# Kernel tuning notes

Hardware: AMD Instinct MI355X
Metric: run time of the kernel (lower is better)

The kernel has to match this reference:

```python
import jax, jax.numpy as jnp
import numpy as np

B, D_IN, D_H = 8192, 1024, 1024


def setup_inputs() -> dict:
    key = jax.random.key(0)
    ks = jax.random.split(key, 11)
    s_in = 1.0 / np.sqrt(D_IN)
    s_h = 1.0 / np.sqrt(D_H)
    return {
        "x": jax.random.normal(ks[0], (B, D_IN), jnp.float32),
        "h": jax.random.normal(ks[1], (B, D_H), jnp.float32),
        "Wiz": jax.random.normal(ks[2], (D_IN, D_H), jnp.float32) * s_in,
        "Uhz": jax.random.normal(ks[3], (D_H, D_H), jnp.float32) * s_h,
        "bz": jax.random.normal(ks[4], (D_H,), jnp.float32) * 0.01,
        "Wir": jax.random.normal(ks[5], (D_IN, D_H), jnp.float32) * s_in,
        "Uhr": jax.random.normal(ks[6], (D_H, D_H), jnp.float32) * s_h,
        "br": jax.random.normal(ks[7], (D_H,), jnp.float32) * 0.01,
        "Win": jax.random.normal(ks[8], (D_IN, D_H), jnp.float32) * s_in,
        "Uhn": jax.random.normal(ks[9], (D_H, D_H), jnp.float32) * s_h,
        "bn": jax.random.normal(ks[10], (D_H,), jnp.float32) * 0.01,
    }


def reference(x, h, Wiz, Uhz, bz, Wir, Uhr, br, Win, Uhn, bn):
    # Concatenate input-side weights into one GEMM for efficiency; math identical.
    Wi = jnp.concatenate([Wiz, Wir, Win], axis=1)          # [D_in, 3H]
    xz, xr, xn = jnp.split(x @ Wi, 3, axis=1)              # each [B, H]
    Uh = jnp.concatenate([Uhz, Uhr], axis=1)               # [H, 2H]
    hz, hr = jnp.split(h @ Uh, 2, axis=1)
    z = jax.nn.sigmoid(xz + hz + bz)
    r = jax.nn.sigmoid(xr + hr + br)
    # Faithful to source: (r * h) @ Uhn, and act1 (sigmoid) for n, not tanh.
    n = jax.nn.sigmoid(xn + (r * h) @ Uhn + bn)
    return (1.0 - z) * h + z * n
```

## Files before the change

### kernel.cpp

```cpp
#include <hip/hip_runtime.h>
#include <hip/hip_bf16.h>

typedef __attribute__((ext_vector_type(8))) short short8;
typedef __attribute__((ext_vector_type(4))) float f32x4;

#define DEV __device__ __forceinline__

DEV float bf2f(unsigned short u) {
    union { unsigned int i; float f; } v;
    v.i = ((unsigned int)u) << 16;
    return v.f;
}
DEV unsigned short f2bf(float f) {
    union { float f; unsigned int i; } v; v.f = f;
    unsigned int r = v.i + 0x7FFFu + ((v.i >> 16) & 1u);
    return (unsigned short)(r >> 16);
}
DEV float sigmoidf_(float x) {
    return 1.0f / (1.0f + __expf(-x));
}

__global__ void conv_xh(const float* __restrict__ x, const float* __restrict__ h,
                        unsigned short* __restrict__ xw, unsigned short* __restrict__ hw,
                        int n)
{
    int i = (blockIdx.x * blockDim.x + threadIdx.x) * 8;
    const float* src; unsigned short* dst; int off;
    if (i < n) { src = x; dst = xw; off = i; }
    else       { src = h; dst = hw; off = i - n; }
    float4 a = *(const float4*)(src + off);
    float4 b = *(const float4*)(src + off + 4);
    union { uint4 v; unsigned short s[8]; } o;
    o.s[0]=f2bf(a.x); o.s[1]=f2bf(a.y); o.s[2]=f2bf(a.z); o.s[3]=f2bf(a.w);
    o.s[4]=f2bf(b.x); o.s[5]=f2bf(b.y); o.s[6]=f2bf(b.z); o.s[7]=f2bf(b.w);
    *(uint4*)(dst + off) = o.v;
}

__global__ void tconv(const float* __restrict__ s0, const float* __restrict__ s1,
                      const float* __restrict__ s2, const float* __restrict__ s3,
                      const float* __restrict__ s4, const float* __restrict__ s5,
                      unsigned short* __restrict__ d0, unsigned short* __restrict__ d1,
                      unsigned short* __restrict__ d2, unsigned short* __restrict__ d3,
                      unsigned short* __restrict__ d4, unsigned short* __restrict__ d5)
{
    __shared__ float lds[32][33];
    const float* src; unsigned short* dst;
    switch (blockIdx.z) {
        case 0: src=s0; dst=d0; break;
        case 1: src=s1; dst=d1; break;
        case 2: src=s2; dst=d2; break;
        case 3: src=s3; dst=d3; break;
        case 4: src=s4; dst=d4; break;
        default: src=s5; dst=d5; break;
    }
    int k0 = blockIdx.x * 32, n0 = blockIdx.y * 32;
    int tx = threadIdx.x & 31, ty = threadIdx.x >> 5;
    #pragma unroll
    for (int i = 0; i < 4; i++)
        lds[ty + 8*i][tx] = src[(size_t)(k0 + ty + 8*i)*1024 + n0 + tx];
    __syncthreads();
    #pragma unroll
    for (int i = 0; i < 4; i++)
        dst[(size_t)(n0 + ty + 8*i)*1024 + k0 + tx] = f2bf(lds[tx][ty + 8*i]);
}

template<int EPI>
__global__ __launch_bounds__(256, 2)
void gemm_bt(const unsigned short* __restrict__ A,
             const unsigned short* __restrict__ Bt,
             unsigned short* __restrict__ Cbf,
             int N, int K,
             const unsigned short* __restrict__ xn, int xnStride,
             const float* __restrict__ bn,
             const float* __restrict__ zbuf,
             const float* __restrict__ hbuf,
             float* __restrict__ out)
{
    __shared__ unsigned short lA[128*32];
    __shared__ unsigned short lB[128*32];
    const int tid = threadIdx.x;
    const int gm = blockIdx.x * 128, gn = blockIdx.y * 128;

    const int w  = tid >> 6, l = tid & 63;
    const int wm = (w >> 1) * 64, wn = (w & 1) * 64;
    const int lr = l & 15, lk = l >> 4;

    f32x4 acc[4][4] = {};

    const int srow = tid >> 2;
    const int scol = (tid & 3) * 8;
    const unsigned short* Ab = A  + (size_t)(gm + srow) * K + scol;
    const unsigned short* Bb = Bt + (size_t)(gn + srow) * K + scol;
    char* lAp = (char*)lA + tid * 16;
    char* lBp = (char*)lB + tid * 16;

    for (int kt = 0; kt < K; kt += 32) {
        __syncthreads();
        __builtin_amdgcn_global_load_lds(
            (const __attribute__((address_space(1))) void*)(Ab + kt),
            (__attribute__((address_space(3))) void*)lAp, 16, 0, 0);
        __builtin_amdgcn_global_load_lds(
            (const __attribute__((address_space(1))) void*)(Ab + kt + (size_t)64*K),
            (__attribute__((address_space(3))) void*)(lAp + 4096), 16, 0, 0);
        __builtin_amdgcn_global_load_lds(
            (const __attribute__((address_space(1))) void*)(Bb + kt),
            (__attribute__((address_space(3))) void*)lBp, 16, 0, 0);
        __builtin_amdgcn_global_load_lds(
            (const __attribute__((address_space(1))) void*)(Bb + kt + (size_t)64*K),
            (__attribute__((address_space(3))) void*)(lBp + 4096), 16, 0, 0);
        __syncthreads();

        short8 af[4], bfr[4];
        #pragma unroll
        for (int mi = 0; mi < 4; mi++)
            af[mi] = *(const short8*)&lA[(wm + mi*16 + lr)*32 + lk*8];
        #pragma unroll
        for (int ni = 0; ni < 4; ni++)
            bfr[ni] = *(const short8*)&lB[(wn + ni*16 + lr)*32 + lk*8];
        #pragma unroll
        for (int mi = 0; mi < 4; mi++)
            #pragma unroll
            for (int ni = 0; ni < 4; ni++)
                acc[mi][ni] = __builtin_amdgcn_mfma_f32_16x16x32_bf16(
                    af[mi], bfr[ni], acc[mi][ni], 0, 0, 0);
    }

    #pragma unroll
    for (int mi = 0; mi < 4; mi++) {
        #pragma unroll
        for (int j = 0; j < 4; j++) {
            int row = gm + wm + mi*16 + lk*4 + j;
            #pragma unroll
            for (int ni = 0; ni < 4; ni++) {
                int col = gn + wn + ni*16 + lr;
                float v = acc[mi][ni][j];
                if (EPI == 0) {
                    Cbf[(size_t)row * N + col] = f2bf(v);
                } else {
                    float pre = v + bf2f(xn[(size_t)row * xnStride + col]) + bn[col];
                    float nv  = sigmoidf_(pre);
                    float zv  = zbuf[(size_t)row * 1024 + col];
                    float hv  = hbuf[(size_t)row * 1024 + col];
                    out[(size_t)row * 1024 + col] = (1.0f - zv) * hv + zv * nv;
                }
            }
        }
    }
}

__global__ void ew1(const unsigned short* __restrict__ xzrn,
                    const unsigned short* __restrict__ hzr,
                    const float* __restrict__ bz, const float* __restrict__ br,
                    const float* __restrict__ h,
                    float* __restrict__ z, unsigned short* __restrict__ rh)
{
    int i = blockIdx.x * blockDim.x + threadIdx.x;
    int r = i >> 7;
    int c = (i & 127) * 8;
    union { uint4 v; unsigned short s[8]; } xz, xr, hz, hr, rho;
    xz.v = *(const uint4*)(xzrn + (size_t)r*3072 + c);
    xr.v = *(const uint4*)(xzrn + (size_t)r*3072 + 1024 + c);
    hz.v = *(const uint4*)(hzr  + (size_t)r*2048 + c);
    hr.v = *(const uint4*)(hzr  + (size_t)r*2048 + 1024 + c);
    float4 h0 = *(const float4*)(h + (size_t)r*1024 + c);
    float4 h1 = *(const float4*)(h + (size_t)r*1024 + c + 4);
    float hv[8]  = {h0.x,h0.y,h0.z,h0.w,h1.x,h1.y,h1.z,h1.w};
    float4 bz0 = *(const float4*)(bz + c), bz1 = *(const float4*)(bz + c + 4);
    float4 br0 = *(const float4*)(br + c), br1 = *(const float4*)(br + c + 4);
    float bzv[8] = {bz0.x,bz0.y,bz0.z,bz0.w,bz1.x,bz1.y,bz1.z,bz1.w};
    float brv[8] = {br0.x,br0.y,br0.z,br0.w,br1.x,br1.y,br1.z,br1.w};
    float zo[8];
    #pragma unroll
    for (int j = 0; j < 8; j++) {
        float zv = sigmoidf_(bf2f(xz.s[j]) + bf2f(hz.s[j]) + bzv[j]);
        zo[j] = zv;
        float rv = sigmoidf_(bf2f(xr.s[j]) + bf2f(hr.s[j]) + brv[j]);
        rho.s[j] = f2bf(rv * hv[j]);
    }
    *(float4*)(z + (size_t)r*1024 + c)     = make_float4(zo[0],zo[1],zo[2],zo[3]);
    *(float4*)(z + (size_t)r*1024 + c + 4) = make_float4(zo[4],zo[5],zo[6],zo[7]);
    *(uint4*)(rh + (size_t)r*1024 + c) = rho.v;
}

extern "C" void kernel_launch(void* const* d_in, const int* in_sizes, int n_in,
                              void* d_out, int out_size, void* d_ws, size_t ws_size,
                              hipStream_t stream)
{
    const float* x   = (const float*)d_in[0];
    const float* h   = (const float*)d_in[1];
    const float* Wiz = (const float*)d_in[2];
    const float* Uhz = (const float*)d_in[3];
    const float* bz  = (const float*)d_in[4];
    const float* Wir = (const float*)d_in[5];
    const float* Uhr = (const float*)d_in[6];
    const float* br  = (const float*)d_in[7];
    const float* Win = (const float*)d_in[8];
    const float* Uhn = (const float*)d_in[9];
    const float* bn  = (const float*)d_in[10];
    float* out = (float*)d_out;

    char* ws = (char*)d_ws;
    const size_t MB = 1024ull * 1024ull;
    unsigned short* xw   = (unsigned short*)(ws + 0);
    unsigned short* hw   = (unsigned short*)(ws + 16*MB);
    unsigned short* W3t  = (unsigned short*)(ws + 32*MB);
    unsigned short* U2t  = (unsigned short*)(ws + 38*MB);
    unsigned short* Unt  = (unsigned short*)(ws + 42*MB);
    unsigned short* xzrn = (unsigned short*)(ws + 44*MB);
    unsigned short* hzr  = (unsigned short*)(ws + 92*MB);
    float*          zbuf = (float*)(ws + 124*MB);
    unsigned short* rh   = (unsigned short*)(ws + 156*MB);

    const int B = 8192, H = 1024;

    conv_xh<<<dim3(2*B*H/8/256), dim3(256), 0, stream>>>(x, h, xw, hw, B*H);

    tconv<<<dim3(32, 32, 6), dim3(256), 0, stream>>>(
        Wiz, Wir, Win, Uhz, Uhr, Uhn,
        W3t, W3t + 1024*1024, W3t + 2*1024*1024, U2t, U2t + 1024*1024, Unt);

    gemm_bt<0><<<dim3(64, 24), dim3(256), 0, stream>>>(
        xw, W3t, xzrn, 3072, 1024, nullptr, 0, nullptr, nullptr, nullptr, nullptr);

    gemm_bt<0><<<dim3(64, 16), dim3(256), 0, stream>>>(
        hw, U2t, hzr, 2048, 1024, nullptr, 0, nullptr, nullptr, nullptr, nullptr);

    ew1<<<dim3(B*H/8/256), dim3(256), 0, stream>>>(xzrn, hzr, bz, br, h, zbuf, rh);

    gemm_bt<1><<<dim3(64, 8), dim3(256), 0, stream>>>(
        rh, Unt, nullptr, 1024, 1024, xzrn + 2048, 3072, bn, zbuf, h, out);
}
```

Before: 312.8 us.

## Concatenate x/h GEMMs along K and fuse gate elementwise into GEMM epilogues

Stacks input and hidden weights along K so z/r pre-activations come from one K=2048 GEMM with sigmoid and r*h computed in the epilogue, removing the separate elementwise kernel. The n gate is similarly computed as one GEMM over [x | r*h] with stacked Win/Uhn, eliminating the bf16 xzrn/hzr intermediates and their round-trip traffic. Total FLOPs stay the same, but launches and global memory traffic shrink; the epilogue now does branchy per-column work.

Measured after the change: 293.5 us. 1.07x faster.

```diff
diff --git a/kernel.cpp b/kernel.cpp
--- a/kernel.cpp
+++ b/kernel.cpp
@@ -36,22 +36,20 @@
     *(uint4*)(dst + off) = o.v;
 }
 
-__global__ void tconv(const float* __restrict__ s0, const float* __restrict__ s1,
-                      const float* __restrict__ s2, const float* __restrict__ s3,
-                      const float* __restrict__ s4, const float* __restrict__ s5,
-                      unsigned short* __restrict__ d0, unsigned short* __restrict__ d1,
-                      unsigned short* __restrict__ d2, unsigned short* __restrict__ d3,
-                      unsigned short* __restrict__ d4, unsigned short* __restrict__ d5)
+__global__ void tconv(const float* __restrict__ Wiz, const float* __restrict__ Uhz,
+                      const float* __restrict__ Wir, const float* __restrict__ Uhr,
+                      const float* __restrict__ Win, const float* __restrict__ Uhn,
+                      unsigned short* __restrict__ B1t, unsigned short* __restrict__ B3t)
 {
     __shared__ float lds[32][33];
     const float* src; unsigned short* dst;
     switch (blockIdx.z) {
-        case 0: src=s0; dst=d0; break;
-        case 1: src=s1; dst=d1; break;
-        case 2: src=s2; dst=d2; break;
-        case 3: src=s3; dst=d3; break;
-        case 4: src=s4; dst=d4; break;
-        default: src=s5; dst=d5; break;
+        case 0: src=Wiz; dst=B1t;                            break;
+        case 1: src=Uhz; dst=B1t + 1024;                     break;
+        case 2: src=Wir; dst=B1t + (size_t)1024*2048;        break;
+        case 3: src=Uhr; dst=B1t + (size_t)1024*2048 + 1024; break;
+        case 4: src=Win; dst=B3t;                            break;
+        default: src=Uhn; dst=B3t + 1024;                    break;
     }
     int k0 = blockIdx.x * 32, n0 = blockIdx.y * 32;
     int tx = threadIdx.x & 31, ty = threadIdx.x >> 5;
@@ -61,19 +59,19 @@
     __syncthreads();
     #pragma unroll
     for (int i = 0; i < 4; i++)
-        dst[(size_t)(n0 + ty + 8*i)*1024 + k0 + tx] = f2bf(lds[tx][ty + 8*i]);
+        dst[(size_t)(n0 + ty + 8*i)*2048 + k0 + tx] = f2bf(lds[tx][ty + 8*i]);
 }
 
 template<int EPI>
 __global__ __launch_bounds__(256, 2)
-void gemm_bt(const unsigned short* __restrict__ A,
+void gemm_bt(const unsigned short* __restrict__ A0,
+             const unsigned short* __restrict__ A1,
              const unsigned short* __restrict__ Bt,
-             unsigned short* __restrict__ Cbf,
-             int N, int K,
-             const unsigned short* __restrict__ xn, int xnStride,
-             const float* __restrict__ bn,
-             const float* __restrict__ zbuf,
-             const float* __restrict__ hbuf,
+             const float* __restrict__ bias0,
+             const float* __restrict__ bias1,
+             const float* __restrict__ hsrc,
+             float* __restrict__ zbuf,
+             unsigned short* __restrict__ rh,
              float* __restrict__ out)
 {
     __shared__ unsigned short lA[128*32];
@@ -89,24 +87,25 @@
 
     const int srow = tid >> 2;
     const int scol = (tid & 3) * 8;
-    const unsigned short* Ab = A  + (size_t)(gm + srow) * K + scol;
-    const unsigned short* Bb = Bt + (size_t)(gn + srow) * K + scol;
     char* lAp = (char*)lA + tid * 16;
     char* lBp = (char*)lB + tid * 16;
 
-    for (int kt = 0; kt < K; kt += 32) {
+    for (int kt = 0; kt < 2048; kt += 32) {
+        const unsigned short* Ab = (kt < 1024 ? A0 : A1)
+                                 + (size_t)(gm + srow) * 1024 + (kt & 1023) + scol;
+        const unsigned short* Bb = Bt + (size_t)(gn + srow) * 2048 + kt + scol;
         __syncthreads();
         __builtin_amdgcn_global_load_lds(
-            (const __attribute__((address_space(1))) void*)(Ab + kt),
+            (const __attribute__((address_space(1))) void*)Ab,
             (__attribute__((address_space(3))) void*)lAp, 16, 0, 0);
         __builtin_amdgcn_global_load_lds(
-            (const __attribute__((address_space(1))) void*)(Ab + kt + (size_t)64*K),
+            (const __attribute__((address_space(1))) void*)(Ab + (size_t)64*1024),
             (__attribute__((address_space(3))) void*)(lAp + 4096), 16, 0, 0);
         __builtin_amdgcn_global_load_lds(
-            (const __attribute__((address_space(1))) void*)(Bb + kt),
+            (const __attribute__((address_space(1))) void*)Bb,
             (__attribute__((address_space(3))) void*)lBp, 16, 0, 0);
         __builtin_amdgcn_global_load_lds(
-            (const __attribute__((address_space(1))) void*)(Bb + kt + (size_t)64*K),
+            (const __attribute__((address_space(1))) void*)(Bb + (size_t)64*2048),
             (__attribute__((address_space(3))) void*)(lBp + 4096), 16, 0, 0);
         __syncthreads();
 
@@ -134,52 +133,24 @@
             for (int ni = 0; ni < 4; ni++) {
                 int col = gn + wn + ni*16 + lr;
                 float v = acc[mi][ni][j];
-                if (EPI == 0) {
-                    Cbf[(size_t)row * N + col] = f2bf(v);
+                if (EPI == 1) {
+                    if (col < 1024) {
+                        zbuf[(size_t)row*1024 + col] = sigmoidf_(v + bias0[col]);
+                    } else {
+                        int c = col - 1024;
+                        float rv = sigmoidf_(v + bias1[c]);
+                        rh[(size_t)row*1024 + c] =
+                            f2bf(rv * hsrc[(size_t)row*1024 + c]);
+                    }
                 } else {
-                    float pre = v + bf2f(xn[(size_t)row * xnStride + col]) + bn[col];
-                    float nv  = sigmoidf_(pre);
-                    float zv  = zbuf[(size_t)row * 1024 + col];
-                    float hv  = hbuf[(size_t)row * 1024 + col];
-                    out[(size_t)row * 1024 + col] = (1.0f - zv) * hv + zv * nv;
+                    float nv = sigmoidf_(v + bias0[col]);
+                    float zv = zbuf[(size_t)row*1024 + col];
+                    float hv = hsrc[(size_t)row*1024 + col];
+                    out[(size_t)row*1024 + col] = (1.0f - zv)*hv + zv*nv;
                 }
             }
         }
     }
-}
-
-__global__ void ew1(const unsigned short* __restrict__ xzrn,
-                    const unsigned short* __restrict__ hzr,
-                    const float* __restrict__ bz, const float* __restrict__ br,
-                    const float* __restrict__ h,
-                    float* __restrict__ z, unsigned short* __restrict__ rh)
-{
-    int i = blockIdx.x * blockDim.x + threadIdx.x;
-    int r = i >> 7;
-    int c = (i & 127) * 8;
-    union { uint4 v; unsigned short s[8]; } xz, xr, hz, hr, rho;
-    xz.v = *(const uint4*)(xzrn + (size_t)r*3072 + c);
-    xr.v = *(const uint4*)(xzrn + (size_t)r*3072 + 1024 + c);
-    hz.v = *(const uint4*)(hzr  + (size_t)r*2048 + c);
-    hr.v = *(const uint4*)(hzr  + (size_t)r*2048 + 1024 + c);
-    float4 h0 = *(const float4*)(h + (size_t)r*1024 + c);
-    float4 h1 = *(const float4*)(h + (size_t)r*1024 + c + 4);
-    float hv[8]  = {h0.x,h0.y,h0.z,h0.w,h1.x,h1.y,h1.z,h1.w};
-    float4 bz0 = *(const float4*)(bz + c), bz1 = *(const float4*)(bz + c + 4);
-    float4 br0 = *(const float4*)(br + c), br1 = *(const float4*)(br + c + 4);
-    float bzv[8] = {bz0.x,bz0.y,bz0.z,bz0.w,bz1.x,bz1.y,bz1.z,bz1.w};
-    float brv[8] = {br0.x,br0.y,br0.z,br0.w,br1.x,br1.y,br1.z,br1.w};
-    float zo[8];
-    #pragma unroll
-    for (int j = 0; j < 8; j++) {
-        float zv = sigmoidf_(bf2f(xz.s[j]) + bf2f(hz.s[j]) + bzv[j]);
-        zo[j] = zv;
-        float rv = sigmoidf_(bf2f(xr.s[j]) + bf2f(hr.s[j]) + brv[j]);
-        rho.s[j] = f2bf(rv * hv[j]);
-    }
-    *(float4*)(z + (size_t)r*1024 + c)     = make_float4(zo[0],zo[1],zo[2],zo[3]);
-    *(float4*)(z + (size_t)r*1024 + c + 4) = make_float4(zo[4],zo[5],zo[6],zo[7]);
-    *(uint4*)(rh + (size_t)r*1024 + c) = rho.v;
 }
 
 extern "C" void kernel_launch(void* const* d_in, const int* in_sizes, int n_in,
@@ -203,30 +174,21 @@
     const size_t MB = 1024ull * 1024ull;
     unsigned short* xw   = (unsigned short*)(ws + 0);
     unsigned short* hw   = (unsigned short*)(ws + 16*MB);
-    unsigned short* W3t  = (unsigned short*)(ws + 32*MB);
-    unsigned short* U2t  = (unsigned short*)(ws + 38*MB);
-    unsigned short* Unt  = (unsigned short*)(ws + 42*MB);
-    unsigned short* xzrn = (unsigned short*)(ws + 44*MB);
-    unsigned short* hzr  = (unsigned short*)(ws + 92*MB);
-    float*          zbuf = (float*)(ws + 124*MB);
-    unsigned short* rh   = (unsigned short*)(ws + 156*MB);
+    unsigned short* B1t  = (unsigned short*)(ws + 32*MB);
+    unsigned short* B3t  = (unsigned short*)(ws + 40*MB);
+    float*          zbuf = (float*)(ws + 44*MB);
+    unsigned short* rh   = (unsigned short*)(ws + 76*MB);
 
     const int B = 8192, H = 1024;
 
     conv_xh<<<dim3(2*B*H/8/256), dim3(256), 0, stream>>>(x, h, xw, hw, B*H);
 
     tconv<<<dim3(32, 32, 6), dim3(256), 0, stream>>>(
-        Wiz, Wir, Win, Uhz, Uhr, Uhn,
-        W3t, W3t + 1024*1024, W3t + 2*1024*1024, U2t, U2t + 1024*1024, Unt);
+        Wiz, Uhz, Wir, Uhr, Win, Uhn, B1t, B3t);
 
-    gemm_bt<0><<<dim3(64, 24), dim3(256), 0, stream>>>(
-        xw, W3t, xzrn, 3072, 1024, nullptr, 0, nullptr, nullptr, nullptr, nullptr);
+    gemm_bt<1><<<dim3(64, 16), dim3(256), 0, stream>>>(
+        xw, hw, B1t, bz, br, h, zbuf, rh, nullptr);
 
-    gemm_bt<0><<<dim3(64, 16), dim3(256), 0, stream>>>(
-        hw, U2t, hzr, 2048, 1024, nullptr, 0, nullptr, nullptr, nullptr, nullptr);
-
-    ew1<<<dim3(B*H/8/256), dim3(256), 0, stream>>>(xzrn, hzr, bz, br, h, zbuf, rh);
-
-    gemm_bt<1><<<dim3(64, 8), dim3(256), 0, stream>>>(
-        rh, Unt, nullptr, 1024, 1024, xzrn + 2048, 3072, bn, zbuf, h, out);
+    gemm_bt<2><<<dim3(64, 8), dim3(256), 0, stream>>>(
+        xw, rh, B3t, bn, nullptr, h, zbuf, nullptr, out);
 }
```
